# Kernel tuning notes

Hardware: AMD Instinct MI355X
Metric: run time of the kernel (lower is better)

## Reference

```python
import jax, jax.numpy as jnp
import numpy as np

# Constants from the torch module
S_DECAY = 0.95    # sentence_decay
P_DECAY = 0.99    # paragraph_decay
D_DECAY = 0.999   # document_decay
ALPHA = 0.1       # delta_update alpha for sentence/paragraph
DOC_ALPHA = 0.05  # delta_update alpha for document
BETA = 1.0
PARA_GROUP = 5    # sentences per paragraph
EPS = 1e-12       # F.normalize eps


def _normalize(x):
    # matches torch.nn.functional.normalize(x, dim=-1)
    return x / jnp.maximum(jnp.linalg.norm(x, axis=-1, keepdims=True), EPS)


def _delta_step(M, kn, v, alpha, beta):
    # M: [H, dk, dv]; kn: [dk] (already L2-normalized); v: [dv]
    # M_new = M @ (I - alpha * kn kn^T) + beta * kn v^T   (erase matrix is symmetric,
    # so the einsum 'hkv,hkj->hjv' form equals this rank-1 update -- no dk x dk matrix needed)
    kTM = jnp.einsum('k,hkv->hv', kn, M)                       # [H, dv]
    return M - alpha * kn[None, :, None] * kTM[:, None, :] \
             + beta * (kn[:, None] * v[None, :])[None, :, :]


def _scan_updates(M0, K, V, decay, alpha, beta):
    # Streaming delta-rule: per step, decay then erase/write.
    def step(M, kv):
        k, v = kv
        M = M * decay
        M = _delta_step(M, _normalize(k), v, alpha, beta)
        return M, None
    M, _ = jax.lax.scan(step, M0, (K, V))
    return M


def setup_inputs() -> dict:
    key = jax.random.key(0)
    ks = jax.random.split(key, 7)
    T, d_emb, d_k, d_v, H = 1000, 768, 256, 256, 8
    emb = jax.random.normal(ks[0], (T, d_emb), dtype=jnp.float32)
    q = jax.random.normal(ks[1], (d_k,), dtype=jnp.float32)
    W_k = jax.random.normal(ks[2], (d_emb, d_k), dtype=jnp.float32) * 0.02
    b_k = jax.random.normal(ks[3], (d_k,), dtype=jnp.float32) * 0.02
    W_v = jax.random.normal(ks[4], (d_emb, d_v), dtype=jnp.float32) * 0.02
    b_v = jax.random.normal(ks[5], (d_v,), dtype=jnp.float32) * 0.02
    M_sent0 = jnp.zeros((H, d_k, d_v), dtype=jnp.float32)
    M_para0 = jnp.zeros((H, d_k, d_v), dtype=jnp.float32)
    M_doc0 = jnp.zeros((H, d_k, d_v), dtype=jnp.float32)
    return {"emb": emb, "q": q, "W_k": W_k, "b_k": b_k, "W_v": W_v, "b_v": b_v,
            "M_sent0": M_sent0, "M_para0": M_para0, "M_doc0": M_doc0}


def reference(emb, q, W_k, b_k, W_v, b_v, M_sent0, M_para0, M_doc0):
    T, d_emb = emb.shape
    # Level 1: sentence memory -- one delta update per sentence embedding
    K = emb @ W_k + b_k            # [T, dk]
    V = emb @ W_v + b_v            # [T, dv]
    M_sent = _scan_updates(M_sent0, K, V, S_DECAY, ALPHA, BETA)
    # Level 2: paragraph memory -- mean of each group of 5 sentence embeddings
    para_emb = emb.reshape(T // PARA_GROUP, PARA_GROUP, d_emb).mean(axis=1)
    PK = para_emb @ W_k + b_k
    PV = para_emb @ W_v + b_v
    M_para = _scan_updates(M_para0, PK, PV, P_DECAY, ALPHA, BETA)
    # Level 3: document memory -- single update from paragraph-memory statistics
    doc_k = M_para.mean(axis=0).mean(axis=-1)   # [dk]
    doc_v = M_para.mean(axis=0).mean(axis=0)    # [dv]
    M_doc = M_doc0 * D_DECAY
    M_doc = _delta_step(M_doc, _normalize(doc_k), doc_v, DOC_ALPHA, BETA)
    # recall(q, level='all')
    qn = _normalize(q)
    def recall(M):
        return jnp.einsum('hkv,k->hv', M, qn).mean(axis=0)   # [dv]
    return 0.2 * recall(M_sent) + 0.3 * recall(M_para) + 0.5 * recall(M_doc)
```

## Files before the change

kernel.cpp:

```cpp
#include <hip/hip_runtime.h>
#include <hip/hip_bf16.h>

#define ALPHA   0.1f
#define S_DECAY 0.95f
#define P_DECAY 0.99f
#define D_EMB   768
#define DK      256

template<int ctrl, int row_mask>
__device__ __forceinline__ float dpp_add(float x) {
    int y = __builtin_amdgcn_update_dpp(0, __float_as_int(x), ctrl, row_mask, 0xF, true);
    return x + __int_as_float(y);
}

template<int N>
__device__ __forceinline__ void wave_allred_arr(float (&x)[N]) {
#pragma unroll
    for (int n = 0; n < N; ++n) x[n] = dpp_add<0xB1,  0xF>(x[n]);
#pragma unroll
    for (int n = 0; n < N; ++n) x[n] = dpp_add<0x4E,  0xF>(x[n]);
#pragma unroll
    for (int n = 0; n < N; ++n) x[n] = dpp_add<0x141, 0xF>(x[n]);
#pragma unroll
    for (int n = 0; n < N; ++n) x[n] = dpp_add<0x140, 0xF>(x[n]);
#pragma unroll
    for (int n = 0; n < N; ++n) x[n] = dpp_add<0x142, 0xA>(x[n]);
#pragma unroll
    for (int n = 0; n < N; ++n) x[n] = dpp_add<0x143, 0xC>(x[n]);
#pragma unroll
    for (int n = 0; n < N; ++n)
        x[n] = __int_as_float(__builtin_amdgcn_readlane(__float_as_int(x[n]), 63));
}

__device__ __forceinline__ float dot4v(const float4& a, const float4& b) {
    float t0 = a.x * b.x; t0 = fmaf(a.y, b.y, t0);
    float t1 = a.z * b.z; t1 = fmaf(a.w, b.w, t1);
    return t0 + t1;
}

__device__ __forceinline__ float rl(float x, int lane) {
    return __int_as_float(__builtin_amdgcn_readlane(__float_as_int(x), lane));
}

__global__ __launch_bounds__(256) void prep_kernel(
    const float* __restrict__ emb,
    const float* __restrict__ Wk, const float* __restrict__ bk,
    const float* __restrict__ Wv, const float* __restrict__ bv,
    float* __restrict__ K, float* __restrict__ V, float* __restrict__ USrev,
    float* __restrict__ out, int T)
{
    const int tid = threadIdx.x;
    const int bid = blockIdx.x;
    const int NBLK = (T / 4) * 2;
    if (bid >= NBLK) {
        const int PADS = ((T + 63) / 64) * 64;
        for (int i = tid; i < (PADS - T) * DK; i += 256) USrev[(size_t)T * DK + i] = 0.f;
        out[tid] = 0.f;
        return;
    }
    const int mat = bid & 1;
    const int r0  = (bid >> 1) * 4;

    __shared__ float se[4][D_EMB];
    __shared__ float s_red[4][4];

    const float4* emb4 = reinterpret_cast<const float4*>(emb);
#pragma unroll
    for (int r = 0; r < 4; ++r) {
        if (tid < D_EMB / 4)
            reinterpret_cast<float4*>(se[r])[tid] = emb4[(size_t)(r0 + r) * (D_EMB / 4) + tid];
    }
    __syncthreads();

    const float* Wp = mat ? Wv : Wk;
    const float* bp = mat ? bv : bk;
    const int j = tid;

    float a0 = 0.f, a1 = 0.f, a2 = 0.f, a3 = 0.f;
    float c0 = Wp[j],        c1 = Wp[j + DK],     c2 = Wp[j + 2*DK], c3 = Wp[j + 3*DK];
    float p0 = Wp[j + 4*DK], p1 = Wp[j + 5*DK],   p2 = Wp[j + 6*DK], p3 = Wp[j + 7*DK];

    for (int d = 0; d < D_EMB; d += 4) {
        int dn = d + 8; if (dn >= D_EMB) dn = 0;
        const float* wn = Wp + (size_t)dn * DK + j;
        float n0 = wn[0], n1 = wn[DK], n2 = wn[2*DK], n3 = wn[3*DK];

        float4 e0 = *reinterpret_cast<const float4*>(&se[0][d]);
        float4 e1 = *reinterpret_cast<const float4*>(&se[1][d]);
        float4 e2 = *reinterpret_cast<const float4*>(&se[2][d]);
        float4 e3 = *reinterpret_cast<const float4*>(&se[3][d]);

        a0 = fmaf(e0.x, c0, a0); a0 = fmaf(e0.y, c1, a0);
        a0 = fmaf(e0.z, c2, a0); a0 = fmaf(e0.w, c3, a0);
        a1 = fmaf(e1.x, c0, a1); a1 = fmaf(e1.y, c1, a1);
        a1 = fmaf(e1.z, c2, a1); a1 = fmaf(e1.w, c3, a1);
        a2 = fmaf(e2.x, c0, a2); a2 = fmaf(e2.y, c1, a2);
        a2 = fmaf(e2.z, c2, a2); a2 = fmaf(e2.w, c3, a2);
        a3 = fmaf(e3.x, c0, a3); a3 = fmaf(e3.y, c1, a3);
        a3 = fmaf(e3.z, c2, a3); a3 = fmaf(e3.w, c3, a3);

        c0 = p0; c1 = p1; c2 = p2; c3 = p3;
        p0 = n0; p1 = n1; p2 = n2; p3 = n3;
    }

    float bj = bp[j];
    float o0 = a0 + bj, o1 = a1 + bj, o2 = a2 + bj, o3 = a3 + bj;
    float* dst = mat ? V : K;
    dst[(size_t)(r0 + 0) * DK + j] = o0;
    dst[(size_t)(r0 + 1) * DK + j] = o1;
    dst[(size_t)(r0 + 2) * DK + j] = o2;
    dst[(size_t)(r0 + 3) * DK + j] = o3;

    if (mat == 0) {
        const int wave = tid >> 6, l = tid & 63;
        float red[4] = { o0*o0, o1*o1, o2*o2, o3*o3 };
        wave_allred_arr(red);
        if (l == 0) {
            s_red[wave][0] = red[0]; s_red[wave][1] = red[1];
            s_red[wave][2] = red[2]; s_red[wave][3] = red[3];
        }
        __syncthreads();
        float t0 = s_red[0][0] + s_red[1][0] + s_red[2][0] + s_red[3][0];
        float t1 = s_red[0][1] + s_red[1][1] + s_red[2][1] + s_red[3][1];
        float t2 = s_red[0][2] + s_red[1][2] + s_red[2][2] + s_red[3][2];
        float t3 = s_red[0][3] + s_red[1][3] + s_red[2][3] + s_red[3][3];
        USrev[(size_t)(T - 1 - (r0 + 0)) * DK + j] = o0 * (1.0f / fmaxf(sqrtf(t0), 1e-12f));
        USrev[(size_t)(T - 1 - (r0 + 1)) * DK + j] = o1 * (1.0f / fmaxf(sqrtf(t1), 1e-12f));
        USrev[(size_t)(T - 1 - (r0 + 2)) * DK + j] = o2 * (1.0f / fmaxf(sqrtf(t2), 1e-12f));
        USrev[(size_t)(T - 1 - (r0 + 3)) * DK + j] = o3 * (1.0f / fmaxf(sqrtf(t3), 1e-12f));
    }
}

#define SU_STRIDE 260
__global__ __launch_bounds__(512) void mid_kernel(
    const float* __restrict__ K, const float* __restrict__ V,
    const float* __restrict__ USrev,
    float* __restrict__ UPrev, float* __restrict__ UPfwd,
    float* __restrict__ PV, float* __restrict__ SVv,
    float* __restrict__ AinvT, float* __restrict__ F1, float* __restrict__ biasF,
    int P, int NCS, int NCP)
{
    __shared__ __align__(16) float sU[64 * SU_STRIDE];
    __shared__ __align__(16) float sA[64 * 65];
    __shared__ float s_pd[64];
    __shared__ float s_sv[64];
    __shared__ float4 s_f1w[4][64];
    float* sX = sU;

    const int tid = threadIdx.x, wv = tid >> 6, l = tid & 63;
    const int bid = blockIdx.x;
    int type, m;
    if (bid < NCS)            { type = 0; m = bid; }
    else if (bid < NCS + NCP) { type = 1; m = bid - NCS; }
    else                      { type = 2; m = bid - NCS - NCP; }

    if (type == 2) {
        if (tid < 64) s_pd[tid] = powf(P_DECAY, (float)tid);
        __syncthreads();
    }

    if (type == 0) {
        const float4* U4 = reinterpret_cast<const float4*>(USrev) + (size_t)m * 4096;
        for (int idx = tid; idx < 4096; idx += 512) {
            float4 t = U4[idx];
            int row = idx >> 6, c4 = (idx & 63) << 2;
            *reinterpret_cast<float4*>(&sU[row * SU_STRIDE + c4]) = t;
        }
    } else if (type == 1) {
        if (tid < 256) {
            const float4* K4 = reinterpret_cast<const float4*>(K);
            for (int ii = 0; ii < 16; ii += 2) {
                const int iA = wv * 16 + ii, iB = iA + 1;
                const int pA = P - 1 - (64 * m + iA);
                const int pB = P - 1 - (64 * m + iB);
                float4 ka[5], kb[5];
                if (pA >= 0) {
#pragma unroll
                    for (int s = 0; s < 5; ++s) ka[s] = K4[(size_t)(5 * pA + s) * 64 + l];
                }
                if (pB >= 0) {
#pragma unroll
                    for (int s = 0; s < 5; ++s) kb[s] = K4[(size_t)(5 * pB + s) * 64 + l];
                }
                {
                    float4 u = make_float4(0.f, 0.f, 0.f, 0.f);
                    if (pA >= 0) {
                        float4 pk = make_float4(0.f, 0.f, 0.f, 0.f);
#pragma unroll
                        for (int s = 0; s < 5; ++s) {
                            pk.x += ka[s].x; pk.y += ka[s].y; pk.z += ka[s].z; pk.w += ka[s].w;
                        }
                        pk.x *= 0.2f; pk.y *= 0.2f; pk.z *= 0.2f; pk.w *= 0.2f;
                        float red[1] = { dot4v(pk, pk) };
                        wave_allred_arr(red);
                        float inv = 1.0f / fmaxf(sqrtf(red[0]), 1e-12f);
                        u = make_float4(pk.x * inv, pk.y * inv, pk.z * inv, pk.w * inv);
                    }
                    *reinterpret_cast<float4*>(&sU[iA * SU_STRIDE + 4 * l]) = u;
                    reinterpret_cast<float4*>(UPrev)[(size_t)(64 * m + iA) * 64 + l] = u;
                }
                {
                    float4 u = make_float4(0.f, 0.f, 0.f, 0.f);
                    if (pB >= 0) {
                        float4 pk = make_float4(0.f, 0.f, 0.f, 0.f);
#pragma unroll
                        for (int s = 0; s < 5; ++s) {
                            pk.x += kb[s].x; pk.y += kb[s].y; pk.z += kb[s].z; pk.w += kb[s].w;
                        }
                        pk.x *= 0.2f; pk.y *= 0.2f; pk.z *= 0.2f; pk.w *= 0.2f;
                        float red[1] = { dot4v(pk, pk) };
                        wave_allred_arr(red);
                        float inv = 1.0f / fmaxf(sqrtf(red[0]), 1e-12f);
                        u = make_float4(pk.x * inv, pk.y * inv, pk.z * inv, pk.w * inv);
                    }
                    *reinterpret_cast<float4*>(&sU[iB * SU_STRIDE + 4 * l]) = u;
                    reinterpret_cast<float4*>(UPrev)[(size_t)(64 * m + iB) * 64 + l] = u;
                }
            }
        }
    } else {
        if (tid < 256) {
            const float4* K4 = reinterpret_cast<const float4*>(K);
            const float4* V4 = reinterpret_cast<const float4*>(V);
            float4 f1p = make_float4(0.f, 0.f, 0.f, 0.f);
            for (int ii = 0; ii < 16; ii += 2) {
                const int iA = wv * 16 + ii, iB = iA + 1;
                const int pA = 64 * m + iA, pB = 64 * m + iB;
                float4 ka[5], va[5], kb[5], vb[5];
                if (pA < P) {
#pragma unroll
                    for (int s = 0; s < 5; ++s) {
                        ka[s] = K4[(size_t)(5 * pA + s) * 64 + l];
                        va[s] = V4[(size_t)(5 * pA + s) * 64 + l];
                    }
                }
                if (pB < P) {
#pragma unroll
                    for (int s = 0; s < 5; ++s) {
                        kb[s] = K4[(size_t)(5 * pB + s) * 64 + l];
                        vb[s] = V4[(size_t)(5 * pB + s) * 64 + l];
                    }
                }
                {
                    float4 u = make_float4(0.f, 0.f, 0.f, 0.f);
                    float sv = 0.f;
                    if (pA < P) {
                        float4 pk = make_float4(0.f, 0.f, 0.f, 0.f);
                        float4 pv = make_float4(0.f, 0.f, 0.f, 0.f);
#pragma unroll
                        for (int s = 0; s < 5; ++s) {
                            pk.x += ka[s].x; pk.y += ka[s].y; pk.z += ka[s].z; pk.w += ka[s].w;
                            pv.x += va[s].x; pv.y += va[s].y; pv.z += va[s].z; pv.w += va[s].w;
                        }
                        pk.x *= 0.2f; pk.y *= 0.2f; pk.z *= 0.2f; pk.w *= 0.2f;
                        pv.x *= 0.2f; pv.y *= 0.2f; pv.z *= 0.2f; pv.w *= 0.2f;
                        reinterpret_cast<float4*>(PV)[(size_t)pA * 64 + l] = pv;
                        float red[2] = { dot4v(pk, pk), pv.x + pv.y + pv.z + pv.w };
                        wave_allred_arr(red);
                        float inv = 1.0f / fmaxf(sqrtf(red[0]), 1e-12f);
                        u = make_float4(pk.x * inv, pk.y * inv, pk.z * inv, pk.w * inv);
                        sv = red[1];
                    }
                    *reinterpret_cast<float4*>(&sU[iA * SU_STRIDE + 4 * l]) = u;
                    reinterpret_cast<float4*>(UPfwd)[(size_t)(64 * m + iA) * 64 + l] = u;
                    if (l == 0) { s_sv[iA] = sv; SVv[64 * m + iA] = sv; }
                    float f = s_pd[63 - iA] * sv;
                    f1p.x = fmaf(f, u.x, f1p.x); f1p.y = fmaf(f, u.y, f1p.y);
                    f1p.z = fmaf(f, u.z, f1p.z); f1p.w = fmaf(f, u.w, f1p.w);
                }
                {
                    float4 u = make_float4(0.f, 0.f, 0.f, 0.f);
                    float sv = 0.f;
                    if (pB < P) {
                        float4 pk = make_float4(0.f, 0.f, 0.f, 0.f);
                        float4 pv = make_float4(0.f, 0.f, 0.f, 0.f);
#pragma unroll
                        for (int s = 0; s < 5; ++s) {
                            pk.x += kb[s].x; pk.y += kb[s].y; pk.z += kb[s].z; pk.w += kb[s].w;
                            pv.x += vb[s].x; pv.y += vb[s].y; pv.z += vb[s].z; pv.w += vb[s].w;
                        }
                        pk.x *= 0.2f; pk.y *= 0.2f; pk.z *= 0.2f; pk.w *= 0.2f;
                        pv.x *= 0.2f; pv.y *= 0.2f; pv.z *= 0.2f; pv.w *= 0.2f;
                        reinterpret_cast<float4*>(PV)[(size_t)pB * 64 + l] = pv;
                        float red[2] = { dot4v(pk, pk), pv.x + pv.y + pv.z + pv.w };
                        wave_allred_arr(red);
                        float inv = 1.0f / fmaxf(sqrtf(red[0]), 1e-12f);
                        u = make_float4(pk.x * inv, pk.y * inv, pk.z * inv, pk.w * inv);
                        sv = red[1];
                    }
                    *reinterpret_cast<float4*>(&sU[iB * SU_STRIDE + 4 * l]) = u;
                    reinterpret_cast<float4*>(UPfwd)[(size_t)(64 * m + iB) * 64 + l] = u;
                    if (l == 0) { s_sv[iB] = sv; SVv[64 * m + iB] = sv; }
                    float f = s_pd[63 - iB] * sv;
                    f1p.x = fmaf(f, u.x, f1p.x); f1p.y = fmaf(f, u.y, f1p.y);
                    f1p.z = fmaf(f, u.z, f1p.z); f1p.w = fmaf(f, u.w, f1p.w);
                }
            }
            s_f1w[wv][l] = f1p;
        }
    }
    __syncthreads();

    if (type == 2 && wv == 0) {
        float4 a = s_f1w[0][l], b = s_f1w[1][l], c = s_f1w[2][l], d = s_f1w[3][l];
        float4 tot = make_float4(a.x+b.x+c.x+d.x, a.y+b.y+c.y+d.y,
                                 a.z+b.z+c.z+d.z, a.w+b.w+c.w+d.w);
        reinterpret_cast<float4*>(F1)[(size_t)m * 64 + l] = tot;
    }

    {
        const int i0 = (tid & 31) * 2;
        const int j0 = (tid >> 5) * 4;
        float g[2][4];
#pragma unroll
        for (int r = 0; r < 2; ++r)
#pragma unroll
            for (int c = 0; c < 4; ++c) g[r][c] = 0.f;
#pragma unroll 4
        for (int k4 = 0; k4 < 64; ++k4) {
            float4 A0 = *reinterpret_cast<const float4*>(&sU[(i0    ) * SU_STRIDE + 4*k4]);
            float4 A1 = *reinterpret_cast<const float4*>(&sU[(i0 + 1) * SU_STRIDE + 4*k4]);
            float4 B0 = *reinterpret_cast<const float4*>(&sU[(j0    ) * SU_STRIDE + 4*k4]);
            float4 B1 = *reinterpret_cast<const float4*>(&sU[(j0 + 1) * SU_STRIDE + 4*k4]);
            float4 B2 = *reinterpret_cast<const float4*>(&sU[(j0 + 2) * SU_STRIDE + 4*k4]);
            float4 B3 = *reinterpret_cast<const float4*>(&sU[(j0 + 3) * SU_STRIDE + 4*k4]);
            g[0][0] += dot4v(A0, B0); g[0][1] += dot4v(A0, B1);
            g[0][2] += dot4v(A0, B2); g[0][3] += dot4v(A0, B3);
            g[1][0] += dot4v(A1, B0); g[1][1] += dot4v(A1, B1);
            g[1][2] += dot4v(A1, B2); g[1][3] += dot4v(A1, B3);
        }
#pragma unroll
        for (int r = 0; r < 2; ++r)
#pragma unroll
            for (int c = 0; c < 4; ++c) {
                int gi = i0 + r, gj = j0 + c;
                float val = 0.f;
                if (gj < gi) {
                    val = ALPHA * g[r][c];
                    if (type == 2) val *= s_pd[gi - gj];
                }
                sA[gi * 65 + gj] = val;
            }
    }
    __syncthreads();

    if (type == 2 && wv == 0) {
        float dotb = 0.f;
#pragma unroll
        for (int jj = 0; jj < 64; ++jj)
            dotb = fmaf(sA[l * 65 + jj], s_sv[jj], dotb);
        biasF[m * 64 + l] = dotb * (1.0f / ALPHA);
    }

    {
        const int base = (wv & 3) * 16;
        float x[16];
#pragma unroll
        for (int r = 0; r < 16; ++r) x[r] = (base + r == l && wv < 4) ? 1.f : 0.f;
        for (int s = 0; s < 4; ++s) {
            if (wv == s) {
#pragma unroll
                for (int i = 1; i < 16; ++i)
#pragma unroll
                    for (int jj = 0; jj < 16; ++jj)
                        if (jj < i)
                            x[i] = fmaf(-sA[(base + i) * 65 + (base + jj)], x[jj], x[i]);
#pragma unroll
                for (int r = 0; r < 16; ++r) sX[(base + r) * 65 + l] = x[r];
            }
            __syncthreads();
            if (wv > s && wv < 4) {
#pragma unroll
                for (int i = 0; i < 16; ++i) {
                    float xi = sX[(s * 16 + i) * 65 + l];
#pragma unroll
                    for (int r = 0; r < 16; ++r)
                        x[r] = fmaf(-sA[(base + r) * 65 + (s * 16 + i)], xi, x[r]);
                }
            }
        }
    }
    __syncthreads();

    float* dstA = AinvT + (size_t)bid * 4096;
    for (int idx = tid; idx < 4096; idx += 512) {
        int jcol = idx >> 6, irow = idx & 63;
        dstA[idx] = sX[irow * 65 + jcol];
    }
}

__global__ __launch_bounds__(512) void accum2_kernel(
    const float* __restrict__ V, const float* __restrict__ PV,
    const float* __restrict__ USrev, const float* __restrict__ UPrev,
    const float* __restrict__ UPfwd, const float* __restrict__ AinvT,
    const float* __restrict__ F1, const float* __restrict__ biasF,
    const float* __restrict__ q,
    float* __restrict__ out, int T, int P, int NCS, int NCP)
{
    __shared__ float s_cp[8][64];
    __shared__ float4 s_part[8][64];
    __shared__ float s_powd[65];
    __shared__ float s_b[64];
    __shared__ float s_cpa[4][64];
    __shared__ float wc[64];
    __shared__ float s_gs[1];

    const int b = blockIdx.x, tid = threadIdx.x;
    const int wave = tid >> 6, l = tid & 63, wb = wave * 8;

    if (tid <= 64) s_powd[tid] = powf(P_DECAY, (float)tid);

    float4 q4 = reinterpret_cast<const float4*>(q)[l];
    float qs[1] = { dot4v(q4, q4) };
    wave_allred_arr(qs);
    float qinv = 1.0f / fmaxf(sqrtf(qs[0]), 1e-12f);
    float4 qn = make_float4(q4.x * qinv, q4.y * qinv, q4.z * qinv, q4.w * qinv);
    __syncthreads();

    int ci, chunk, realN; const float* src; float decay;
    if (b < NCS)              { ci = b;             chunk = b;        src = V;  decay = S_DECAY; realN = T; }
    else if (b < NCS + NCP)   { ci = b - NCS;       chunk = NCS + ci; src = PV; decay = P_DECAY; realN = P; }
    else                      { ci = b - NCS - NCP; chunk = NCS + ci; src = PV; decay = P_DECAY; realN = P; }

    float xr[16];
    {
        const int part = (tid & 255) >> 6, k = tid & 63;
        const float* Xc = AinvT + (size_t)chunk * 4096;
#pragma unroll
        for (int jj = 0; jj < 16; ++jj)
            xr[jj] = Xc[(part * 16 + jj) * 64 + k];
    }

    {
        const float4* U4; const float* Xb; float4 w1;
        if (b < NCS) {
            U4 = reinterpret_cast<const float4*>(USrev); Xb = AinvT; w1 = qn;
        } else if (b < NCS + NCP) {
            U4 = reinterpret_cast<const float4*>(UPrev); Xb = AinvT + (size_t)NCS * 4096; w1 = qn;
        } else {
            U4 = reinterpret_cast<const float4*>(UPrev); Xb = AinvT + (size_t)NCS * 4096;
            w1 = make_float4(1.f, 1.f, 1.f, 1.f);
        }
        float4 curU[8]; float curX[8];
#pragma unroll
        for (int r = 0; r < 8; ++r) {
            curU[r] = U4[(size_t)(wb + r) * 64 + l];
            curX[r] = Xb[(size_t)(wb + r) * 64 + l];
        }
        for (int m = 0; m <= ci; ++m) {
            float4 nxtU[8]; float nxtX[8];
            if (m + 1 <= ci) {
#pragma unroll
                for (int r = 0; r < 8; ++r) {
                    nxtU[r] = U4[(size_t)(m + 1) * 4096 + (size_t)(wb + r) * 64 + l];
                    nxtX[r] = Xb[(size_t)(m + 1) * 4096 + (size_t)(wb + r) * 64 + l];
                }
            }
            float d[8];
#pragma unroll
            for (int r = 0; r < 8; ++r) d[r] = dot4v(curU[r], w1);
            wave_allred_arr(d);
            if (m == ci) {
                if (l == 0) {
#pragma unroll
                    for (int r = 0; r < 8; ++r) s_b[wb + r] = d[r];
                }
                break;
            }
            float cp = 0.f;
#pragma unroll
            for (int r = 0; r < 8; ++r) cp = fmaf(curX[r], d[r], cp);
            s_cp[wave][l] = cp;
            __syncthreads();
            float cl = 0.f;
#pragma unroll
            for (int w = 0; w < 8; ++w) cl += s_cp[w][l];
            float4 part = make_float4(0.f, 0.f, 0.f, 0.f);
#pragma unroll
            for (int r = 0; r < 8; ++r) {
                float cw = rl(cl, wb + r);
                part.x = fmaf(cw, curU[r].x, part.x); part.y = fmaf(cw, curU[r].y, part.y);
                part.z = fmaf(cw, curU[r].z, part.z); part.w = fmaf(cw, curU[r].w, part.w);
            }
            s_part[wave][l] = part;
            __syncthreads();
            float4 s = make_float4(0.f, 0.f, 0.f, 0.f);
#pragma unroll
            for (int w = 0; w < 8; ++w) {
                float4 p = s_part[w][l];
                s.x += p.x; s.y += p.y; s.z += p.z; s.w += p.w;
            }
            w1.x = fmaf(-ALPHA, s.x, w1.x); w1.y = fmaf(-ALPHA, s.y, w1.y);
            w1.z = fmaf(-ALPHA, s.z, w1.z); w1.w = fmaf(-ALPHA, s.w, w1.w);
#pragma unroll
            for (int r = 0; r < 8; ++r) { curU[r] = nxtU[r]; curX[r] = nxtX[r]; }
        }
    }
    __syncthreads();

    if (b >= NCS + NCP) {
        float4 y = make_float4(0.f, 0.f, 0.f, 0.f);
        const float4* Uf4 = reinterpret_cast<const float4*>(UPfwd);
        float4 cU[8]; float cX[8];
#pragma unroll
        for (int r = 0; r < 8; ++r) {
            cU[r] = Uf4[(size_t)(wb + r) * 64 + l];
            cX[r] = AinvT[(size_t)(NCS + NCP) * 4096 + (size_t)(wb + r) * 64 + l];
        }
        for (int mm = 0; mm < NCP; ++mm) {
            float4 nU[8]; float nX[8];
            if (mm + 1 < NCP) {
#pragma unroll
                for (int r = 0; r < 8; ++r) {
                    nU[r] = Uf4[(size_t)(mm + 1) * 4096 + (size_t)(wb + r) * 64 + l];
                    nX[r] = AinvT[(size_t)(NCS + NCP + mm + 1) * 4096 + (size_t)(wb + r) * 64 + l];
                }
            }
            float biasr[8];
#pragma unroll
            for (int r = 0; r < 8; ++r) biasr[r] = biasF[mm * 64 + wb + r];
            float4 f1 = reinterpret_cast<const float4*>(F1)[(size_t)mm * 64 + l];
            float d[8];
#pragma unroll
            for (int r = 0; r < 8; ++r) d[r] = dot4v(cU[r], y);
            wave_allred_arr(d);
#pragma unroll
            for (int r = 0; r < 8; ++r)
                d[r] = fmaf(s_powd[wb + r + 1], d[r], biasr[r]);
            float cp = 0.f;
#pragma unroll
            for (int r = 0; r < 8; ++r) cp = fmaf(cX[r], d[r], cp);
            s_cp[wave][l] = cp;
            __syncthreads();
            float cl = 0.f;
#pragma unroll
            for (int w = 0; w < 8; ++w) cl += s_cp[w][l];
            float4 part = make_float4(0.f, 0.f, 0.f, 0.f);
#pragma unroll
            for (int r = 0; r < 8; ++r) {
                float cw = s_powd[63 - (wb + r)] * rl(cl, wb + r);
                part.x = fmaf(cw, cU[r].x, part.x); part.y = fmaf(cw, cU[r].y, part.y);
                part.z = fmaf(cw, cU[r].z, part.z); part.w = fmaf(cw, cU[r].w, part.w);
            }
            s_part[wave][l] = part;
            __syncthreads();
            float4 s = make_float4(0.f, 0.f, 0.f, 0.f);
#pragma unroll
            for (int w = 0; w < 8; ++w) {
                float4 p = s_part[w][l];
                s.x += p.x; s.y += p.y; s.z += p.z; s.w += p.w;
            }
            float d64 = s_powd[64];
            y.x = fmaf(d64, y.x, fmaf(-ALPHA, s.x, f1.x));
            y.y = fmaf(d64, y.y, fmaf(-ALPHA, s.y, f1.y));
            y.z = fmaf(d64, y.z, fmaf(-ALPHA, s.z, f1.z));
            y.w = fmaf(d64, y.w, fmaf(-ALPHA, s.w, f1.w));
            if (mm + 1 < NCP) {
#pragma unroll
                for (int r = 0; r < 8; ++r) { cU[r] = nU[r]; cX[r] = nX[r]; }
            }
        }
        float fin[2] = { dot4v(y, y), dot4v(qn, y) };
        wave_allred_arr(fin);
        if (tid == 0) s_gs[0] = fin[1] / fmaxf(sqrtf(fin[0]), 2.56e-10f);
        __syncthreads();
    }

    if (tid < 256) {
        const int part = tid >> 6, k = tid & 63;
        float cp = 0.f;
#pragma unroll
        for (int jj = 0; jj < 16; ++jj) {
            int j = part * 16 + jj;
            cp = fmaf(xr[jj], s_b[j], cp);
        }
        s_cpa[part][k] = cp;
    }
    __syncthreads();
    if (tid < 64) {
        float c = s_cpa[0][tid] + s_cpa[1][tid] + s_cpa[2][tid] + s_cpa[3][tid];
        wc[tid] = powf(decay, (float)(ci * 64 + tid)) * c;
    }
    __syncthreads();
    if (tid < 256) {
        const int k = tid;
        float acc = 0.f;
        for (int ii = 0; ii < 64; ++ii) {
            int i = ci * 64 + ii;
            if (i < realN)
                acc = fmaf(wc[ii], src[(size_t)(realN - 1 - i) * DK + k], acc);
        }
        float wlev;
        if (b < NCS)            wlev = 0.2f;
        else if (b < NCS + NCP) wlev = 0.3f;
        else                    wlev = (0.5f / 256.0f) * s_gs[0];
        atomicAdd(&out[k], wlev * acc);
    }
}

extern "C" void kernel_launch(void* const* d_in, const int* in_sizes, int n_in,
                              void* d_out, int out_size, void* d_ws, size_t ws_size,
                              hipStream_t stream) {
    const float* emb = (const float*)d_in[0];
    const float* q   = (const float*)d_in[1];
    const float* Wk  = (const float*)d_in[2];
    const float* bk  = (const float*)d_in[3];
    const float* Wv  = (const float*)d_in[4];
    const float* bv  = (const float*)d_in[5];

    const int T = in_sizes[0] / D_EMB;
    const int P = T / 5;
    const int NCS  = (T + 63) / 64;
    const int NCP  = (P + 63) / 64;
    const int PADS = NCS * 64;
    const int PADP = NCP * 64;
    const int NCH  = NCS + 2 * NCP;

    float* ws    = (float*)d_ws;
    float* K     = ws;
    float* V     = K     + (size_t)T * DK;
    float* PV    = V     + (size_t)T * DK;
    float* USrev = PV    + (size_t)PADP * DK;
    float* UPrev = USrev + (size_t)PADS * DK;
    float* UPfwd = UPrev + (size_t)PADP * DK;
    float* SVv   = UPfwd + (size_t)PADP * DK;
    float* AinvT = SVv   + PADP;
    float* F1    = AinvT + (size_t)NCH * 4096;
    float* biasF = F1    + (size_t)NCP * 256;

    prep_kernel<<<(T / 4) * 2 + 1, 256, 0, stream>>>(emb, Wk, bk, Wv, bv,
                                                     K, V, USrev, (float*)d_out, T);
    mid_kernel<<<NCH, 512, 0, stream>>>(K, V, USrev, UPrev, UPfwd, PV, SVv,
                                        AinvT, F1, biasF, P, NCS, NCP);
    accum2_kernel<<<NCH, 512, 0, stream>>>(V, PV, USrev, UPrev, UPfwd, AinvT,
                                           F1, biasF, q, (float*)d_out, T, P, NCS, NCP);
}
```

Measured before the change: 174.8 us.

## Replace cross-wave partial reductions with redundant per-wave compute in chunk accumulation

Each chunk iteration of the accumulation loops now publishes only the 64 reduced d values to shared memory, with one barrier per step instead of two. Every wave then redundantly computes the full 64-wide X·d product from a register-resident 64-element X column and the full U·cl contraction, reloading all 64 U rows from global memory. This removes the s_cp/s_part shared-memory round trips and one barrier per step. In exchange it multiplies per-wave global loads and FMAs by 8, and adds heavy register pressure from the 64-float xall array plus 8 float4 loads per group.

```diff
diff --git a/kernel.cpp b/kernel.cpp
--- a/kernel.cpp
+++ b/kernel.cpp
@@ -397,8 +397,7 @@
     const float* __restrict__ q,
     float* __restrict__ out, int T, int P, int NCS, int NCP)
 {
-    __shared__ float s_cp[8][64];
-    __shared__ float4 s_part[8][64];
+    __shared__ float s_d[2][64];
     __shared__ float s_powd[65];
     __shared__ float s_b[64];
     __shared__ float s_cpa[4][64];
@@ -423,8 +422,8 @@
     else                      { ci = b - NCS - NCP; chunk = NCS + ci; src = PV; decay = P_DECAY; realN = P; }
 
     float xr[16];
-    {
-        const int part = (tid & 255) >> 6, k = tid & 63;
+    if (tid < 256) {
+        const int part = tid >> 6, k = tid & 63;
         const float* Xc = AinvT + (size_t)chunk * 4096;
 #pragma unroll
         for (int jj = 0; jj < 16; ++jj)
@@ -441,21 +440,17 @@
             U4 = reinterpret_cast<const float4*>(UPrev); Xb = AinvT + (size_t)NCS * 4096;
             w1 = make_float4(1.f, 1.f, 1.f, 1.f);
         }
-        float4 curU[8]; float curX[8];
-#pragma unroll
-        for (int r = 0; r < 8; ++r) {
+        float4 curU[8];
+#pragma unroll
+        for (int r = 0; r < 8; ++r)
             curU[r] = U4[(size_t)(wb + r) * 64 + l];
-            curX[r] = Xb[(size_t)(wb + r) * 64 + l];
+        float xall[64];
+        if (ci > 0) {
+#pragma unroll
+            for (int j = 0; j < 64; ++j) xall[j] = Xb[(size_t)j * 64 + l];
         }
         for (int m = 0; m <= ci; ++m) {
-            float4 nxtU[8]; float nxtX[8];
-            if (m + 1 <= ci) {
-#pragma unroll
-                for (int r = 0; r < 8; ++r) {
-                    nxtU[r] = U4[(size_t)(m + 1) * 4096 + (size_t)(wb + r) * 64 + l];
-                    nxtX[r] = Xb[(size_t)(m + 1) * 4096 + (size_t)(wb + r) * 64 + l];
-                }
-            }
+            const size_t base = (size_t)m * 4096;
             float d[8];
 #pragma unroll
             for (int r = 0; r < 8; ++r) d[r] = dot4v(curU[r], w1);
@@ -467,33 +462,49 @@
                 }
                 break;
             }
-            float cp = 0.f;
-#pragma unroll
-            for (int r = 0; r < 8; ++r) cp = fmaf(curX[r], d[r], cp);
-            s_cp[wave][l] = cp;
+            if (l == 0) {
+#pragma unroll
+                for (int r = 0; r < 8; ++r) s_d[m & 1][wb + r] = d[r];
+            }
+            float4 nxtU[8];
+#pragma unroll
+            for (int r = 0; r < 8; ++r)
+                nxtU[r] = U4[(size_t)(m + 1) * 4096 + (size_t)(wb + r) * 64 + l];
             __syncthreads();
             float cl = 0.f;
 #pragma unroll
-            for (int w = 0; w < 8; ++w) cl += s_cp[w][l];
-            float4 part = make_float4(0.f, 0.f, 0.f, 0.f);
-#pragma unroll
-            for (int r = 0; r < 8; ++r) {
-                float cw = rl(cl, wb + r);
-                part.x = fmaf(cw, curU[r].x, part.x); part.y = fmaf(cw, curU[r].y, part.y);
-                part.z = fmaf(cw, curU[r].z, part.z); part.w = fmaf(cw, curU[r].w, part.w);
-            }
-            s_part[wave][l] = part;
-            __syncthreads();
+            for (int g = 0; g < 8; ++g) {
+                float cp = 0.f;
+#pragma unroll
+                for (int r = 0; r < 8; ++r)
+                    cp = fmaf(xall[g * 8 + r], s_d[m & 1][g * 8 + r], cp);
+                cl += cp;
+            }
             float4 s = make_float4(0.f, 0.f, 0.f, 0.f);
 #pragma unroll
-            for (int w = 0; w < 8; ++w) {
-                float4 p = s_part[w][l];
-                s.x += p.x; s.y += p.y; s.z += p.z; s.w += p.w;
+            for (int g = 0; g < 8; ++g) {
+                float4 ug[8];
+#pragma unroll
+                for (int r = 0; r < 8; ++r)
+                    ug[r] = U4[base + (size_t)(g * 8 + r) * 64 + l];
+                float4 part = make_float4(0.f, 0.f, 0.f, 0.f);
+#pragma unroll
+                for (int r = 0; r < 8; ++r) {
+                    float cw = rl(cl, g * 8 + r);
+                    part.x = fmaf(cw, ug[r].x, part.x); part.y = fmaf(cw, ug[r].y, part.y);
+                    part.z = fmaf(cw, ug[r].z, part.z); part.w = fmaf(cw, ug[r].w, part.w);
+                }
+                s.x += part.x; s.y += part.y; s.z += part.z; s.w += part.w;
             }
             w1.x = fmaf(-ALPHA, s.x, w1.x); w1.y = fmaf(-ALPHA, s.y, w1.y);
             w1.z = fmaf(-ALPHA, s.z, w1.z); w1.w = fmaf(-ALPHA, s.w, w1.w);
 #pragma unroll
-            for (int r = 0; r < 8; ++r) { curU[r] = nxtU[r]; curX[r] = nxtX[r]; }
+            for (int r = 0; r < 8; ++r) curU[r] = nxtU[r];
+            if (m + 1 < ci) {
+#pragma unroll
+                for (int j = 0; j < 64; ++j)
+                    xall[j] = Xb[(size_t)(m + 1) * 4096 + (size_t)j * 64 + l];
+            }
         }
     }
     __syncthreads();
@@ -501,21 +512,16 @@
     if (b >= NCS + NCP) {
         float4 y = make_float4(0.f, 0.f, 0.f, 0.f);
         const float4* Uf4 = reinterpret_cast<const float4*>(UPfwd);
-        float4 cU[8]; float cX[8];
-#pragma unroll
-        for (int r = 0; r < 8; ++r) {
+        float4 cU[8];
+#pragma unroll
+        for (int r = 0; r < 8; ++r)
             cU[r] = Uf4[(size_t)(wb + r) * 64 + l];
-            cX[r] = AinvT[(size_t)(NCS + NCP) * 4096 + (size_t)(wb + r) * 64 + l];
-        }
+        float xall[64];
+#pragma unroll
+        for (int j = 0; j < 64; ++j)
+            xall[j] = AinvT[(size_t)(NCS + NCP) * 4096 + (size_t)j * 64 + l];
         for (int mm = 0; mm < NCP; ++mm) {
-            float4 nU[8]; float nX[8];
-            if (mm + 1 < NCP) {
-#pragma unroll
-                for (int r = 0; r < 8; ++r) {
-                    nU[r] = Uf4[(size_t)(mm + 1) * 4096 + (size_t)(wb + r) * 64 + l];
-                    nX[r] = AinvT[(size_t)(NCS + NCP + mm + 1) * 4096 + (size_t)(wb + r) * 64 + l];
-                }
-            }
+            const size_t ubase = (size_t)mm * 4096;
             float biasr[8];
 #pragma unroll
             for (int r = 0; r < 8; ++r) biasr[r] = biasF[mm * 64 + wb + r];
@@ -527,28 +533,42 @@
 #pragma unroll
             for (int r = 0; r < 8; ++r)
                 d[r] = fmaf(s_powd[wb + r + 1], d[r], biasr[r]);
-            float cp = 0.f;
-#pragma unroll
-            for (int r = 0; r < 8; ++r) cp = fmaf(cX[r], d[r], cp);
-            s_cp[wave][l] = cp;
+            if (l == 0) {
+#pragma unroll
+                for (int r = 0; r < 8; ++r) s_d[mm & 1][wb + r] = d[r];
+            }
+            float4 nU[8];
+            if (mm + 1 < NCP) {
+#pragma unroll
+                for (int r = 0; r < 8; ++r)
+                    nU[r] = Uf4[(size_t)(mm + 1) * 4096 + (size_t)(wb + r) * 64 + l];
+            }
             __syncthreads();
             float cl = 0.f;
 #pragma unroll
-            for (int w = 0; w < 8; ++w) cl += s_cp[w][l];
-            float4 part = make_float4(0.f, 0.f, 0.f, 0.f);
-#pragma unroll
-            for (int r = 0; r < 8; ++r) {
-                float cw = s_powd[63 - (wb + r)] * rl(cl, wb + r);
-                part.x = fmaf(cw, cU[r].x, part.x); part.y = fmaf(cw, cU[r].y, part.y);
-                part.z = fmaf(cw, cU[r].z, part.z); part.w = fmaf(cw, cU[r].w, part.w);
-            }
-            s_part[wave][l] = part;
-            __syncthreads();
+            for (int g = 0; g < 8; ++g) {
+                float cp = 0.f;
+#pragma unroll
+                for (int r = 0; r < 8; ++r)
+                    cp = fmaf(xall[g * 8 + r], s_d[mm & 1][g * 8 + r], cp);
+                cl += cp;
+            }
             float4 s = make_float4(0.f, 0.f, 0.f, 0.f);
 #pragma unroll
-            for (int w = 0; w < 8; ++w) {
-                float4 p = s_part[w][l];
-                s.x += p.x; s.y += p.y; s.z += p.z; s.w += p.w;
+            for (int g = 0; g < 8; ++g) {
+                float4 ug[8];
+#pragma unroll
+                for (int r = 0; r < 8; ++r)
+                    ug[r] = Uf4[ubase + (size_t)(g * 8 + r) * 64 + l];
+                float4 part = make_float4(0.f, 0.f, 0.f, 0.f);
+#pragma unroll
+                for (int r = 0; r < 8; ++r) {
+                    const int j = g * 8 + r;
+                    float cw = s_powd[63 - j] * rl(cl, j);
+                    part.x = fmaf(cw, ug[r].x, part.x); part.y = fmaf(cw, ug[r].y, part.y);
+                    part.z = fmaf(cw, ug[r].z, part.z); part.w = fmaf(cw, ug[r].w, part.w);
+                }
+                s.x += part.x; s.y += part.y; s.z += part.z; s.w += part.w;
             }
             float d64 = s_powd[64];
             y.x = fmaf(d64, y.x, fmaf(-ALPHA, s.x, f1.x));
@@ -557,7 +577,10 @@
             y.w = fmaf(d64, y.w, fmaf(-ALPHA, s.w, f1.w));
             if (mm + 1 < NCP) {
 #pragma unroll
-                for (int r = 0; r < 8; ++r) { cU[r] = nU[r]; cX[r] = nX[r]; }
+                for (int r = 0; r < 8; ++r) cU[r] = nU[r];
+#pragma unroll
+                for (int j = 0; j < 64; ++j)
+                    xall[j] = AinvT[(size_t)(NCS + NCP + mm + 1) * 4096 + (size_t)j * 64 + l];
             }
         }
         float fin[2] = { dot4v(y, y), dot4v(qn, y) };
```

New measurement: 632.1 us. 3.62x slower.

## Replace block barriers with per-wave sequence flags and double-buffered LDS in accum2

Applied to the files above, without the earlier changes.

The __syncthreads barriers in both serial chunk loops of accum2_kernel are replaced with per-wave sequence counters in LDS. Each wave publishes with release atomics and spin-waits with acquire loads and s_sleep, while the s_cp and s_part buffers are double-buffered by iteration parity. The xr register preload is dropped and read from global memory at the end, which lowers register pressure. The goal is to cut barrier cost on the latency-bound sequential recurrence, at the cost of spin-polling overhead. The double buffering relies on the second flag wait to keep waves from running more than one iteration ahead.

```diff
diff --git a/kernel.cpp b/kernel.cpp
--- a/kernel.cpp
+++ b/kernel.cpp
@@ -40,6 +40,20 @@
 
 __device__ __forceinline__ float rl(float x, int lane) {
     return __int_as_float(__builtin_amdgcn_readlane(__float_as_int(x), lane));
+}
+
+__device__ __forceinline__ void seq_publish(int* seqp, int v) {
+    __hip_atomic_store(seqp, v, __ATOMIC_RELEASE, __HIP_MEMORY_SCOPE_WORKGROUP);
+}
+__device__ __forceinline__ void seq_wait_all(int* seq, int v) {
+    for (;;) {
+        int ok = 1;
+#pragma unroll
+        for (int w = 0; w < 8; ++w)
+            ok &= (__hip_atomic_load(&seq[w], __ATOMIC_ACQUIRE, __HIP_MEMORY_SCOPE_WORKGROUP) >= v);
+        if (ok) break;
+        __builtin_amdgcn_s_sleep(1);
+    }
 }
 
 __global__ __launch_bounds__(256) void prep_kernel(
@@ -397,8 +411,9 @@
     const float* __restrict__ q,
     float* __restrict__ out, int T, int P, int NCS, int NCP)
 {
-    __shared__ float s_cp[8][64];
-    __shared__ float4 s_part[8][64];
+    __shared__ float s_cp[2][8][64];
+    __shared__ float4 s_part[2][8][64];
+    __shared__ int  seqA[8], seqB[8], seqC[8], seqD[8];
     __shared__ float s_powd[65];
     __shared__ float s_b[64];
     __shared__ float s_cpa[4][64];
@@ -408,6 +423,7 @@
     const int b = blockIdx.x, tid = threadIdx.x;
     const int wave = tid >> 6, l = tid & 63, wb = wave * 8;
 
+    if (tid < 8) { seqA[tid] = 0; seqB[tid] = 0; seqC[tid] = 0; seqD[tid] = 0; }
     if (tid <= 64) s_powd[tid] = powf(P_DECAY, (float)tid);
 
     float4 q4 = reinterpret_cast<const float4*>(q)[l];
@@ -421,15 +437,6 @@
     if (b < NCS)              { ci = b;             chunk = b;        src = V;  decay = S_DECAY; realN = T; }
     else if (b < NCS + NCP)   { ci = b - NCS;       chunk = NCS + ci; src = PV; decay = P_DECAY; realN = P; }
     else                      { ci = b - NCS - NCP; chunk = NCS + ci; src = PV; decay = P_DECAY; realN = P; }
-
-    float xr[16];
-    {
-        const int part = (tid & 255) >> 6, k = tid & 63;
-        const float* Xc = AinvT + (size_t)chunk * 4096;
-#pragma unroll
-        for (int jj = 0; jj < 16; ++jj)
-            xr[jj] = Xc[(part * 16 + jj) * 64 + k];
-    }
 
     {
         const float4* U4; const float* Xb; float4 w1;
@@ -470,11 +477,12 @@
             float cp = 0.f;
 #pragma unroll
             for (int r = 0; r < 8; ++r) cp = fmaf(curX[r], d[r], cp);
-            s_cp[wave][l] = cp;
-            __syncthreads();
+            s_cp[m & 1][wave][l] = cp;
+            if (l == 0) seq_publish(&seqA[wave], m + 1);
+            seq_wait_all(seqA, m + 1);
             float cl = 0.f;
 #pragma unroll
-            for (int w = 0; w < 8; ++w) cl += s_cp[w][l];
+            for (int w = 0; w < 8; ++w) cl += s_cp[m & 1][w][l];
             float4 part = make_float4(0.f, 0.f, 0.f, 0.f);
 #pragma unroll
             for (int r = 0; r < 8; ++r) {
@@ -482,12 +490,13 @@
                 part.x = fmaf(cw, curU[r].x, part.x); part.y = fmaf(cw, curU[r].y, part.y);
                 part.z = fmaf(cw, curU[r].z, part.z); part.w = fmaf(cw, curU[r].w, part.w);
             }
-            s_part[wave][l] = part;
-            __syncthreads();
+            s_part[m & 1][wave][l] = part;
+            if (l == 0) seq_publish(&seqB[wave], m + 1);
+            seq_wait_all(seqB, m + 1);
             float4 s = make_float4(0.f, 0.f, 0.f, 0.f);
 #pragma unroll
             for (int w = 0; w < 8; ++w) {
-                float4 p = s_part[w][l];
+                float4 p = s_part[m & 1][w][l];
                 s.x += p.x; s.y += p.y; s.z += p.z; s.w += p.w;
             }
             w1.x = fmaf(-ALPHA, s.x, w1.x); w1.y = fmaf(-ALPHA, s.y, w1.y);
@@ -530,11 +539,12 @@
             float cp = 0.f;
 #pragma unroll
             for (int r = 0; r < 8; ++r) cp = fmaf(cX[r], d[r], cp);
-            s_cp[wave][l] = cp;
-            __syncthreads();
+            s_cp[mm & 1][wave][l] = cp;
+            if (l == 0) seq_publish(&seqC[wave], mm + 1);
+            seq_wait_all(seqC, mm + 1);
             float cl = 0.f;
 #pragma unroll
-            for (int w = 0; w < 8; ++w) cl += s_cp[w][l];
+            for (int w = 0; w < 8; ++w) cl += s_cp[mm & 1][w][l];
             float4 part = make_float4(0.f, 0.f, 0.f, 0.f);
 #pragma unroll
             for (int r = 0; r < 8; ++r) {
@@ -542,12 +552,13 @@
                 part.x = fmaf(cw, cU[r].x, part.x); part.y = fmaf(cw, cU[r].y, part.y);
                 part.z = fmaf(cw, cU[r].z, part.z); part.w = fmaf(cw, cU[r].w, part.w);
             }
-            s_part[wave][l] = part;
-            __syncthreads();
+            s_part[mm & 1][wave][l] = part;
+            if (l == 0) seq_publish(&seqD[wave], mm + 1);
+            seq_wait_all(seqD, mm + 1);
             float4 s = make_float4(0.f, 0.f, 0.f, 0.f);
 #pragma unroll
             for (int w = 0; w < 8; ++w) {
-                float4 p = s_part[w][l];
+                float4 p = s_part[mm & 1][w][l];
                 s.x += p.x; s.y += p.y; s.z += p.z; s.w += p.w;
             }
             float d64 = s_powd[64];
@@ -568,11 +579,12 @@
 
     if (tid < 256) {
         const int part = tid >> 6, k = tid & 63;
+        const float* Xc = AinvT + (size_t)chunk * 4096;
         float cp = 0.f;
 #pragma unroll
         for (int jj = 0; jj < 16; ++jj) {
             int j = part * 16 + jj;
-            cp = fmaf(xr[jj], s_b[j], cp);
+            cp = fmaf(Xc[j * 64 + k], s_b[j], cp);
         }
         s_cpa[part][k] = cp;
     }
```

New measurement: 182.5 us. +4.4%, slower.
